# Kernel optimization log

Measured on AMD Instinct MI355X. Metric: run time of the kernel, lower is better.

Reference implementation:

```python
import jax, jax.numpy as jnp
import numpy as np

NC = 3
NA = 3
NO2D = NC + 5
BIN = 2
NO3D = BIN * 3 + 3
STRIDES = (8.0, 16.0, 32.0)
ANCHORS = np.array([[10, 13, 16, 30, 33, 23],
                    [30, 61, 62, 45, 59, 119],
                    [116, 90, 156, 198, 373, 326]], np.float32).reshape(3, NA, 2)
IN_CHES = (256, 512, 1024)
SIZES = ((80, 80), (40, 40), (20, 20))
BS = 8


def _conv(x, w, b, pad):
    y = jax.lax.conv_general_dilated(x, w, (1, 1), ((pad, pad), (pad, pad)),
                                     dimension_numbers=('NCHW', 'OIHW', 'NCHW'))
    return y + b[None, :, None, None]


def setup_inputs() -> dict:
    key = jax.random.key(0)
    d = {}
    k = [0]
    def nk():
        k[0] += 1
        return jax.random.fold_in(key, k[0])
    for i, (c, (ny, nx)) in enumerate(zip(IN_CHES, SIZES)):
        d[f"f{i}"] = jax.random.normal(nk(), (BS, c, ny, nx), jnp.float32)
        d[f"w2a{i}"] = jax.random.normal(nk(), (c, c, 3, 3), jnp.float32) * 0.01
        d[f"b2a{i}"] = jnp.zeros((c,), jnp.float32)
        d[f"w2b{i}"] = jax.random.normal(nk(), (NA * NO2D, c, 1, 1), jnp.float32) * 0.01
        d[f"b2b{i}"] = jnp.zeros((NA * NO2D,), jnp.float32)
        d[f"w3a{i}"] = jax.random.normal(nk(), (c, c, 3, 3), jnp.float32) * 0.01
        d[f"b3a{i}"] = jnp.zeros((c,), jnp.float32)
        d[f"w3b{i}"] = jax.random.normal(nk(), (NA * NO3D, c, 1, 1), jnp.float32) * 0.01
        d[f"b3b{i}"] = jnp.zeros((NA * NO3D,), jnp.float32)
    return d


def _decode(feats, params):
    anchors = jnp.asarray(ANCHORS)  # [L, NA, 2]
    preds = []
    for i in range(3):
        x = feats[i]
        w2a, b2a, w2b, b2b, w3a, b3a, w3b, b3b = params[i]
        # detection heads: 3x3 conv -> 1x1 conv
        h2 = _conv(_conv(x, w2a, b2a, 1), w2b, b2b, 0)  # [bs, na*NO2D, ny, nx]
        h3 = _conv(_conv(x, w3a, b3a, 1), w3b, b3b, 0)  # [bs, na*NO3D, ny, nx]
        bs, _, ny, nx = h2.shape
        h2 = h2.reshape(bs, NA, NO2D, ny, nx).transpose(0, 1, 3, 4, 2)  # [bs,na,ny,nx,NO2D]
        h3 = h3.reshape(bs, NA, NO3D, ny, nx).transpose(0, 1, 3, 4, 2).reshape(bs, -1, NO3D)
        # 2d decode
        p2 = jax.nn.sigmoid(h2)
        yv, xv = jnp.meshgrid(jnp.arange(ny, dtype=jnp.float32),
                              jnp.arange(nx, dtype=jnp.float32), indexing='ij')
        grid = jnp.stack((xv, yv), -1)[None, None]  # [1,1,ny,nx,2]
        xy = (p2[..., 0:2] * 2.0 - 0.5 + grid) * STRIDES[i]
        wh = (p2[..., 2:4] * 2.0) ** 2 * anchors[i][None, :, None, None, :]
        p2 = jnp.concatenate([xy, wh, p2[..., 4:]], -1).reshape(bs, -1, NO2D)
        # 3d decode: bin confidences raw, bin orients L2-normalized, dims sigmoid*2-1
        bins = h3[..., :BIN]
        orient = h3[..., BIN:3 * BIN].reshape(bs, -1, BIN, 2)
        norm = jnp.maximum(jnp.linalg.norm(orient, axis=-1, keepdims=True), 1e-12)
        orient = (orient / norm).reshape(bs, -1, BIN * 2)
        dims = jax.nn.sigmoid(h3[..., -3:]) * 2.0 - 1.0
        p3 = jnp.concatenate([bins, orient, dims], -1)
        preds.append(jnp.concatenate([p2, p3], -1))
    return jnp.concatenate(preds, 1)  # [bs, 25200, NO2D+NO3D]


def reference(f0, f1, f2,
              w2a0, b2a0, w2b0, b2b0, w3a0, b3a0, w3b0, b3b0,
              w2a1, b2a1, w2b1, b2b1, w3a1, b3a1, w3b1, b3b1,
              w2a2, b2a2, w2b2, b2b2, w3a2, b3a2, w3b2, b3b2):
    feats = (f0, f1, f2)
    params = ((w2a0, b2a0, w2b0, b2b0, w3a0, b3a0, w3b0, b3b0),
              (w2a1, b2a1, w2b1, b2b1, w3a1, b3a1, w3b1, b3b1),
              (w2a2, b2a2, w2b2, b2b2, w3a2, b3a2, w3b2, b3b2))
    return _decode(feats, params)
```

## Files before the change

kernel.cpp:

```cpp
#include <hip/hip_runtime.h>
#include <hip/hip_bf16.h>
#include <cstddef>
#include <cstdint>
#include <climits>

#define TOT_ANCH 25200

typedef __bf16 bf16x8 __attribute__((ext_vector_type(8)));
typedef float f32x4 __attribute__((ext_vector_type(4)));

__device__ __forceinline__ float sig_(float x) { return 1.0f / (1.0f + __expf(-x)); }

__device__ __forceinline__ short f2bf(float v) {
  return (short)__builtin_bit_cast(unsigned short, __float2bfloat16(v));
}
__device__ __forceinline__ float bf2f(short v) {
  unsigned int u = ((unsigned int)(unsigned short)v) << 16;
  return __builtin_bit_cast(float, u);
}
__device__ __forceinline__ bf16x8 as_bf16x8(int4 v) { return __builtin_bit_cast(bf16x8, v); }

__device__ __forceinline__ void gload_lds16(const void* g, void* l) {
  __builtin_amdgcn_global_load_lds((const __attribute__((address_space(1))) void*)g,
                                   (__attribute__((address_space(3))) void*)l, 16, 0, 0);
}

__device__ const float d_anch[3][3][2] = {
    {{10.f, 13.f}, {16.f, 30.f}, {33.f, 23.f}},
    {{30.f, 61.f}, {62.f, 45.f}, {59.f, 119.f}},
    {{116.f, 90.f}, {156.f, 198.f}, {373.f, 326.f}}};

struct TrP {
  const float* f; short* fb; int C, HW, ptiles, c32, blk0;
};
struct WtP {
  const float* w; short* dst; long CC, MC, off0; int blk0;
};
struct WcP {
  const float* w2b; const float* w3b; short* wc; int csh2, blk0;
};
struct ConvP {
  const short* fb; const short* wt; const float* bA; const float* bB; short* h;
  int C, H, W, HW, Ng, nb_m, nwg, mfast, blk0;
};
struct DeP {
  const short* h; const short* wc; const float* bb2; const float* bb3;
  int C2, H, W, b0, loff, ptiles, lvl, blk0; float stride;
};

__global__ __launch_bounds__(256) void aux_mega(TrP T0, TrP T1, TrP T2,
                                                WtP J0, WtP J1, WtP J2,
                                                WtP J3, WtP J4, WtP J5, int wt_blk0) {
  __shared__ short tile[32][33];
  int bid = blockIdx.x;
  if (bid >= wt_blk0) {
    WtP J = bid >= J5.blk0 ? J5 : bid >= J4.blk0 ? J4 : bid >= J3.blk0 ? J3 :
            bid >= J2.blk0 ? J2 : bid >= J1.blk0 ? J1 : J0;
    long oi = (long)(bid - J.blk0) * 256 + threadIdx.x;
    if (oi >= J.CC) return;
#pragma unroll
    for (int t = 0; t < 9; ++t) J.dst[t * J.MC + J.off0 + oi] = f2bf(J.w[oi * 9 + t]);
    return;
  }
  TrP T = bid >= T2.blk0 ? T2 : (bid >= T1.blk0 ? T1 : T0);
  int l = bid - T.blk0;
  const int pt = l % T.ptiles; l /= T.ptiles;
  const int cg = l % T.c32;
  const int b = l / T.c32;
  const int p0 = pt * 32, c0 = cg * 32, HW = T.HW, C = T.C;
  const int t = threadIdx.x;
  {
    int cl = t >> 3, pl = (t & 7) * 4;
    int pr = p0 + pl;
    if (pr > HW - 4) pr = HW - 4;
    const float4 v = *(const float4*)(T.f + ((long)b * C + c0 + cl) * HW + pr);
    tile[cl][pl + 0] = f2bf(v.x);
    tile[cl][pl + 1] = f2bf(v.y);
    tile[cl][pl + 2] = f2bf(v.z);
    tile[cl][pl + 3] = f2bf(v.w);
  }
  __syncthreads();
  {
    int pl = t >> 3, cl = (t & 7) * 4;
    int pp = p0 + pl;
    if (pp < HW) {
      int k = pl >> 2;
      int start = p0 + 4 * k;
      if (start > HW - 4) start = HW - 4;
      int col = (start - p0) + (pp - start);
      short4 o;
      o.x = tile[cl + 0][col];
      o.y = tile[cl + 1][col];
      o.z = tile[cl + 2][col];
      o.w = tile[cl + 3][col];
      *(short4*)(T.fb + ((long)b * HW + pp) * C + c0 + cl) = o;
    }
  }
}

__global__ __launch_bounds__(256) void wc_prep(WcP K0, WcP K1, WcP K2) {
  int bid = blockIdx.x;
  WcP K = bid >= K2.blk0 ? K2 : (bid >= K1.blk0 ? K1 : K0);
  int idx = (bid - K.blk0) * 256 + threadIdx.x;
  const int C2 = 1 << K.csh2;
  if (idx >= 64 * C2) return;
  const int row = idx >> K.csh2;
  const int c = idx & (C2 - 1);
  const int C = C2 >> 1;
  float v = 0.f;
  if (row < 24) {
    if (c < C) v = K.w2b[row * C + c];
  } else if (row < 51) {
    if (c >= C) v = K.w3b[(row - 24) * C + (c - C)];
  }
  K.wc[idx] = f2bf(v);
}

__global__ __launch_bounds__(512) void conv3x3_mega(ConvP P0, ConvP P1, ConvP P2,
                                                    const short* zbuf) {
  __shared__ __align__(16) short As[2][2][256 * 32];
  __shared__ __align__(16) short Xs[2][2][256 * 32];

  int bid = blockIdx.x;
  ConvP P = bid >= P2.blk0 ? P2 : (bid >= P1.blk0 ? P1 : P0);
  const int C = P.C, H = P.H, W = P.W, HW = P.HW, Ng = P.Ng;
  const int nb_m = P.nb_m, nwg = P.nwg;

  const int orig = bid - P.blk0;
  int wg;
  if (nwg & 7) wg = orig;
  else { const int q = nwg >> 3; wg = (orig & 7) * q + (orig >> 3); }
  int m, n;
  if (P.mfast) { m = wg % nb_m; n = wg / nb_m; }
  else         { const int nb_n = nwg / nb_m; n = wg % nb_n; m = wg / nb_n; }
  const int mt0 = m * 256;
  const int nt0 = n * 256;
  const int M2 = nb_m * 256;

  const int tid = threadIdx.x;
  const int lane = tid & 63;
  const int wave = tid >> 6;
  const int wm = wave >> 2;
  const int wn = wave & 3;

  const int srow0 = tid >> 2;
  const int swzc = ((tid & 3) ^ ((tid >> 3) & 3)) * 8;
  int xs_x[2], xs_y[2], xs_vld[2];
  long xs_base[2], as_base[2];
#pragma unroll
  for (int r = 0; r < 2; ++r) {
    int row = r * 128 + srow0;
    int nn = nt0 + row;
    int vld = nn < Ng;
    int nnc = vld ? nn : 0;
    int b = nnc / HW; int p = nnc - b * HW;
    int y = p / W;    int x = p - y * W;
    xs_x[r] = x; xs_y[r] = y; xs_vld[r] = vld;
    xs_base[r] = (long)((b * H + y) * W + x) * C + swzc;
    as_base[r] = (long)(mt0 + row) * C + swzc;
  }

  f32x4 acc[8][4];
#pragma unroll
  for (int a_ = 0; a_ < 8; ++a_)
#pragma unroll
    for (int b_ = 0; b_ < 4; ++b_) acc[a_][b_] = (f32x4){0.f, 0.f, 0.f, 0.f};

  const int nkb = C >> 6;
  const int nkt = nkb * 9;
  const long MC = (long)M2 * C;
  const short* gzb = zbuf + swzc;

  auto SA = [&](int db, int kh, const short* wtap, int kb64) {
#pragma unroll
    for (int r = 0; r < 2; ++r)
      gload_lds16(wtap + as_base[r] + kb64 + kh * 32,
                  (char*)&As[db][kh][0] + r * 8192 + tid * 16);
  };
  auto SX = [&](int db, int kh, int dy, int dx, int doff) {
#pragma unroll
    for (int r = 0; r < 2; ++r) {
      bool ok = xs_vld[r] && ((unsigned)(xs_y[r] + dy) < (unsigned)H) &&
                ((unsigned)(xs_x[r] + dx) < (unsigned)W);
      const short* gx = ok ? P.fb + xs_base[r] + doff + kh * 32 : gzb;
      gload_lds16(gx, (char*)&Xs[db][kh][0] + r * 8192 + tid * 16);
    }
  };

  {
    const int doff0 = (-W - 1) * C;
    SA(0, 0, P.wt, 0);
    SX(0, 0, -1, -1, doff0);
    SA(0, 1, P.wt, 0);
    SX(0, 1, -1, -1, doff0);
  }

  int ntt = 1, nkb64 = 0;
  for (int kt = 0; kt < nkt; ++kt) {
    const int cur = kt & 1;
    const int nxt = cur ^ 1;
    const bool hasn = (kt + 1) < nkt;
    const int td3 = ntt / 3;
    const int dyn = td3 - 1, dxn = ntt - td3 * 3 - 1;
    const int doffn = (dyn * W + dxn) * C + nkb64;
    const short* wtapn = P.wt + (long)ntt * MC;

    bf16x8 xf[4];
#pragma unroll
    for (int ph = 0; ph < 4; ++ph) {
      const int ks = ph >> 1, mh = ph & 1;
      if (mh == 0) {
        asm volatile("s_waitcnt vmcnt(4)" ::: "memory");
        __builtin_amdgcn_sched_barrier(0);
        __builtin_amdgcn_s_barrier();
      }
      if (hasn) {
        if (ph == 0)      SA(nxt, 0, wtapn, nkb64);
        else if (ph == 1) SX(nxt, 0, dyn, dxn, doffn);
        else if (ph == 2) SA(nxt, 1, wtapn, nkb64);
        else              SX(nxt, 1, dyn, dxn, doffn);
      }
      const char* Ah = (const char*)&As[cur][ks][0];
      const char* Xh = (const char*)&Xs[cur][ks][0];
      if (mh == 0) {
#pragma unroll
        for (int nf = 0; nf < 4; ++nf) {
          int rl = wn * 64 + nf * 16 + (lane & 15);
          int c = (lane >> 4) ^ ((rl >> 1) & 3);
          xf[nf] = as_bf16x8(*(const int4*)(Xh + rl * 64 + c * 16));
        }
      }
      bf16x8 af[4];
#pragma unroll
      for (int mf = 0; mf < 4; ++mf) {
        int rl = wm * 128 + mh * 64 + mf * 16 + (lane & 15);
        int c = (lane >> 4) ^ ((rl >> 1) & 3);
        af[mf] = as_bf16x8(*(const int4*)(Ah + rl * 64 + c * 16));
      }
      asm volatile("s_waitcnt lgkmcnt(0)" ::: "memory");
      __builtin_amdgcn_sched_barrier(0);
      __builtin_amdgcn_s_setprio(1);
#pragma unroll
      for (int mf = 0; mf < 4; ++mf)
#pragma unroll
        for (int nf = 0; nf < 4; ++nf)
          acc[mh * 4 + mf][nf] = __builtin_amdgcn_mfma_f32_16x16x32_bf16(
              af[mf], xf[nf], acc[mh * 4 + mf][nf], 0, 0, 0);
      __builtin_amdgcn_s_setprio(0);
    }
    if (++ntt == 9) { ntt = 0; nkb64 += 64; }
  }

  long nbase[4]; int nok[4];
#pragma unroll
  for (int nf = 0; nf < 4; ++nf) {
    int nn = nt0 + wn * 64 + nf * 16 + (lane & 15);
    nok[nf] = nn < Ng;
    int nnc = nok[nf] ? nn : 0;
    int nb = nnc / HW;
    int np = nnc - nb * HW;
    nbase[nf] = ((long)nb * HW + np) * M2;
  }
#pragma unroll
  for (int g = 0; g < 8; ++g) {
    int co0 = mt0 + wm * 128 + (g >> 2) * 64 + (g & 3) * 16 + (lane >> 4) * 4;
    float bv[4];
#pragma unroll
    for (int rg = 0; rg < 4; ++rg) {
      int co = co0 + rg;
      bv[rg] = co < C ? P.bA[co] : P.bB[co - C];
    }
#pragma unroll
    for (int nf = 0; nf < 4; ++nf) {
      if (nok[nf]) {
        short4 o;
        o.x = f2bf(acc[g][nf][0] + bv[0]);
        o.y = f2bf(acc[g][nf][1] + bv[1]);
        o.z = f2bf(acc[g][nf][2] + bv[2]);
        o.w = f2bf(acc[g][nf][3] + bv[3]);
        *(short4*)(P.h + nbase[nf] + co0) = o;
      }
    }
  }
}

__global__ __launch_bounds__(256) void decode_v3(DeP D0, DeP D1, DeP D2,
                                                 float* __restrict__ out) {
  __shared__ __align__(16) short htileT[32][136];
  __shared__ __align__(16) short Wtile[64][136];
  __shared__ float otile[32][52];
  int bid = blockIdx.x;
  DeP D = bid >= D2.blk0 ? D2 : (bid >= D1.blk0 ? D1 : D0);
  int l = bid - D.blk0;
  const int pt = l % D.ptiles;
  const int bl = l / D.ptiles;
  const int C2 = D.C2, H = D.H, W = D.W, HW = H * W;
  const int t = threadIdx.x;
  const int lane = t & 63;
  const int wv = t >> 6;
  const int p0 = pt * 32;

  const short* hB = D.h + (long)bl * HW * C2;

  f32x4 acc[2];
  acc[0] = (f32x4){0.f, 0.f, 0.f, 0.f};
  acc[1] = (f32x4){0.f, 0.f, 0.f, 0.f};

  const int rounds = C2 >> 7;
  for (int rd = 0; rd < rounds; ++rd) {
    const int c0 = rd << 7;
#pragma unroll
    for (int r = 0; r < 2; ++r) {
      int idx = r * 256 + t;
      int px = idx >> 4, kc = idx & 15;
      int p = p0 + px;
      int pc = p < HW ? p : HW - 1;
      int4 v = *(const int4*)(hB + (long)pc * C2 + c0 + kc * 8);
      *(int4*)&htileT[px][kc * 8] = v;
    }
#pragma unroll
    for (int r = 0; r < 4; ++r) {
      int idx = r * 256 + t;
      int row = idx >> 4, kc = idx & 15;
      int4 v = *(const int4*)(D.wc + (long)row * C2 + c0 + kc * 8);
      *(int4*)&Wtile[row][kc * 8] = v;
    }
    __syncthreads();
#pragma unroll
    for (int st = 0; st < 4; ++st) {
      const int k0 = st * 32 + (lane >> 4) * 8;
      bf16x8 af = as_bf16x8(*(const int4*)&Wtile[wv * 16 + (lane & 15)][k0]);
#pragma unroll
      for (int nf = 0; nf < 2; ++nf) {
        bf16x8 xf = as_bf16x8(*(const int4*)&htileT[nf * 16 + (lane & 15)][k0]);
        acc[nf] = __builtin_amdgcn_mfma_f32_16x16x32_bf16(af, xf, acc[nf], 0, 0, 0);
      }
    }
    __syncthreads();
  }

#pragma unroll
  for (int nf = 0; nf < 2; ++nf) {
    int px = nf * 16 + (lane & 15);
#pragma unroll
    for (int rg = 0; rg < 4; ++rg) {
      int row = wv * 16 + (lane >> 4) * 4 + rg;
      if (row < 51) otile[px][row] = acc[nf][rg];
    }
  }
  __syncthreads();

  if (t < 96) {
    const int pxx = t / 3, a = t - (t / 3) * 3;
    const int p = p0 + pxx;
    if (p < HW) {
      float* o = out + ((size_t)(D.b0 + bl) * TOT_ANCH + D.loff + (size_t)a * HW + p) * 17;
      {
        const int y = p / W, x = p - (p / W) * W;
        float h0 = otile[pxx][a * 8 + 0] + D.bb2[a * 8 + 0];
        float h1 = otile[pxx][a * 8 + 1] + D.bb2[a * 8 + 1];
        float h2 = otile[pxx][a * 8 + 2] + D.bb2[a * 8 + 2];
        float h3 = otile[pxx][a * 8 + 3] + D.bb2[a * 8 + 3];
        float s0 = sig_(h0);
        float s1 = sig_(h1);
        float sw = sig_(h2) * 2.f;
        float sh = sig_(h3) * 2.f;
        o[0] = (s0 * 2.f - 0.5f + (float)x) * D.stride;
        o[1] = (s1 * 2.f - 0.5f + (float)y) * D.stride;
        o[2] = sw * sw * d_anch[D.lvl][a][0];
        o[3] = sh * sh * d_anch[D.lvl][a][1];
        o[4] = sig_(otile[pxx][a * 8 + 4] + D.bb2[a * 8 + 4]);
        o[5] = sig_(otile[pxx][a * 8 + 5] + D.bb2[a * 8 + 5]);
        o[6] = sig_(otile[pxx][a * 8 + 6] + D.bb2[a * 8 + 6]);
        o[7] = sig_(otile[pxx][a * 8 + 7] + D.bb2[a * 8 + 7]);
      }
      {
        float v0 = otile[pxx][24 + a * 9 + 0] + D.bb3[a * 9 + 0];
        float v1 = otile[pxx][24 + a * 9 + 1] + D.bb3[a * 9 + 1];
        float v2 = otile[pxx][24 + a * 9 + 2] + D.bb3[a * 9 + 2];
        float v3 = otile[pxx][24 + a * 9 + 3] + D.bb3[a * 9 + 3];
        float v4 = otile[pxx][24 + a * 9 + 4] + D.bb3[a * 9 + 4];
        float v5 = otile[pxx][24 + a * 9 + 5] + D.bb3[a * 9 + 5];
        float v6 = otile[pxx][24 + a * 9 + 6] + D.bb3[a * 9 + 6];
        float v7 = otile[pxx][24 + a * 9 + 7] + D.bb3[a * 9 + 7];
        float v8 = otile[pxx][24 + a * 9 + 8] + D.bb3[a * 9 + 8];
        float n0 = fmaxf(sqrtf(v2 * v2 + v3 * v3), 1e-12f);
        float n1 = fmaxf(sqrtf(v4 * v4 + v5 * v5), 1e-12f);
        o[8] = v0;
        o[9] = v1;
        o[10] = v2 / n0;
        o[11] = v3 / n0;
        o[12] = v4 / n1;
        o[13] = v5 / n1;
        o[14] = sig_(v6) * 2.f - 1.f;
        o[15] = sig_(v7) * 2.f - 1.f;
        o[16] = sig_(v8) * 2.f - 1.f;
      }
    }
  }
}


static inline size_t al256(size_t x) { return (x + 255) & ~(size_t)255; }

extern "C" void kernel_launch(void* const* d_in, const int* in_sizes, int n_in,
                              void* d_out, int out_size, void* d_ws, size_t ws_size,
                              hipStream_t stream) {
  (void)in_sizes; (void)n_in; (void)out_size;
  char* ws = (char*)d_ws;
  float* out = (float*)d_out;

  hipMemsetAsync(ws, 0, 256, stream);
  const short* zb = (const short*)ws;

  struct Lvl { int C, H, W, loff; float stride; };
  const Lvl L[3] = {{256, 80, 80, 0, 8.f}, {512, 40, 40, 19200, 16.f},
                    {1024, 20, 20, 24000, 32.f}};
  const int B = 8;
  const int ord[3] = {2, 1, 0};

  const float* f_[3]; const float *w2a_[3], *b2a_[3], *w2b_[3], *b2b_[3];
  const float *w3a_[3], *b3a_[3], *w3b_[3], *b3b_[3];
  int HW_[3], ptiles_[3], c32_[3], nbm_[3], mfast_[3], csh2_[3];
  long CC_[3];
  size_t fbB_[3], wtB_[3], hB_[3], wcB_[3];
  for (int i = 0; i < 3; ++i) {
    f_[i]   = (const float*)d_in[9 * i + 0];
    w2a_[i] = (const float*)d_in[9 * i + 1];
    b2a_[i] = (const float*)d_in[9 * i + 2];
    w2b_[i] = (const float*)d_in[9 * i + 3];
    b2b_[i] = (const float*)d_in[9 * i + 4];
    w3a_[i] = (const float*)d_in[9 * i + 5];
    b3a_[i] = (const float*)d_in[9 * i + 6];
    w3b_[i] = (const float*)d_in[9 * i + 7];
    b3b_[i] = (const float*)d_in[9 * i + 8];
    const int C = L[i].C;
    HW_[i] = L[i].H * L[i].W;
    ptiles_[i] = (HW_[i] + 31) / 32;
    c32_[i] = C / 32;
    nbm_[i] = (2 * C) / 256;
    CC_[i] = (long)C * C;
    csh2_[i] = (C == 256) ? 9 : (C == 512) ? 10 : 11;
    fbB_[i] = (size_t)B * HW_[i] * C * 2;
    wtB_[i] = (size_t)36 * CC_[i];
    hB_[i]  = (size_t)B * HW_[i] * 2 * C * 2;
    wcB_[i] = (size_t)64 * 2 * C * 2;
    mfast_[i] = ((size_t)B * HW_[i] * C >= (size_t)18 * CC_[i]) ? 1 : 0;
  }

  size_t off = 256;
  size_t fb_o[3], wt_o[3], h_o[3], wc_o[3];
  for (int i = 0; i < 3; ++i) { fb_o[i] = off; off += al256(fbB_[i]); }
  for (int i = 0; i < 3; ++i) { wt_o[i] = off; off += al256(wtB_[i]); }
  for (int i = 0; i < 3; ++i) { wc_o[i] = off; off += al256(wcB_[i]); }
  for (int i = 0; i < 3; ++i) { h_o[i] = off; off += al256(hB_[i]); }

  if (off <= ws_size) {
    short* fb[3]; short* wtb[3]; short* hb[3]; short* wcb[3];
    for (int i = 0; i < 3; ++i) {
      fb[i] = (short*)(ws + fb_o[i]);
      wtb[i] = (short*)(ws + wt_o[i]);
      hb[i] = (short*)(ws + h_o[i]);
      wcb[i] = (short*)(ws + wc_o[i]);
    }
    TrP T[3]; int tb = 0;
    for (int i = 0; i < 3; ++i) {
      T[i] = TrP{f_[i], fb[i], L[i].C, HW_[i], ptiles_[i], c32_[i], tb};
      tb += ptiles_[i] * c32_[i] * B;
    }
    WtP J[6]; int jb = tb;
    for (int i = 0; i < 3; ++i) {
      J[2 * i]     = WtP{w2a_[i], wtb[i], CC_[i], 2 * CC_[i], 0, jb};
      jb += (int)(CC_[i] / 256);
      J[2 * i + 1] = WtP{w3a_[i], wtb[i], CC_[i], 2 * CC_[i], CC_[i], jb};
      jb += (int)(CC_[i] / 256);
    }
    aux_mega<<<jb, 256, 0, stream>>>(T[0], T[1], T[2], J[0], J[1], J[2], J[3], J[4],
                                     J[5], tb);
    WcP K[3]; int kb = 0;
    for (int i = 0; i < 3; ++i) {
      K[i] = WcP{w2b_[i], w3b_[i], wcb[i], csh2_[i], kb};
      kb += (64 * 2 * L[i].C) / 256;
    }
    wc_prep<<<kb, 256, 0, stream>>>(K[0], K[1], K[2]);

    ConvP P[3]; int cb = 0;
    for (int k = 0; k < 3; ++k) {
      const int i = ord[k];
      const int Ng = B * HW_[i];
      const int ntn = (Ng + 255) / 256;
      const int nwg = ntn * nbm_[i];
      P[k] = ConvP{fb[i], wtb[i], b2a_[i], b3a_[i], hb[i],
                   L[i].C, L[i].H, L[i].W, HW_[i], Ng, nbm_[i], nwg, mfast_[i], cb};
      cb += nwg;
    }
    conv3x3_mega<<<cb, 512, 0, stream>>>(P[0], P[1], P[2], zb);

    DeP D[3]; int db = 0;
    for (int k = 0; k < 3; ++k) {
      const int i = ord[k];
      D[k] = DeP{hb[i], wcb[i], b2b_[i], b3b_[i], 2 * L[i].C, L[i].H, L[i].W,
                 0, L[i].loff, ptiles_[i], i, db, L[i].stride};
      db += ptiles_[i] * B;
    }
    decode_v3<<<db, 256, 0, stream>>>(D[0], D[1], D[2], out);
    return;
  }

  for (int i = 0; i < 3; ++i) {
    const int C = L[i].C, HW = HW_[i];
    int Bg = B;
    for (int cand = 1; cand <= 8; cand <<= 1) {
      int bg = B / cand;
      size_t need = 256 + al256((size_t)bg * HW * C * 2) + al256(wtB_[i]) +
                    al256(wcB_[i]) + (size_t)bg * HW * 2 * C * 2;
      if (need <= ws_size) { Bg = bg; break; }
    }
    size_t fo = 256;
    size_t wo = fo + al256((size_t)Bg * HW * C * 2);
    size_t co = wo + al256(wtB_[i]);
    size_t ho = co + al256(wcB_[i]);
    short* fb = (short*)(ws + fo);
    short* wtb = (short*)(ws + wo);
    short* wcb = (short*)(ws + co);
    short* hb = (short*)(ws + ho);

    TrP TZ{};
    WtP J0 = WtP{w2a_[i], wtb, CC_[i], 2 * CC_[i], 0, 0};
    WtP J1 = WtP{w3a_[i], wtb, CC_[i], 2 * CC_[i], CC_[i], (int)(CC_[i] / 256)};
    WtP JX = J1; JX.blk0 = INT_MAX;
    aux_mega<<<(int)(2 * CC_[i] / 256), 256, 0, stream>>>(TZ, TZ, TZ, J0, J1, JX, JX,
                                                          JX, JX, 0);
    WcP K0 = WcP{w2b_[i], w3b_[i], wcb, csh2_[i], 0};
    WcP KX = K0; KX.blk0 = INT_MAX;
    wc_prep<<<(64 * 2 * C) / 256, 256, 0, stream>>>(K0, KX, KX);

    const int nbg = B / Bg;
    for (int g = 0; g < nbg; ++g) {
      const int b0 = g * Bg;
      TrP T0 = TrP{f_[i] + (size_t)b0 * C * HW, fb, C, HW, ptiles_[i], c32_[i], 0};
      TrP TX = T0; TX.blk0 = INT_MAX;
      WtP JZ{}; JZ.blk0 = INT_MAX;
      aux_mega<<<ptiles_[i] * c32_[i] * Bg, 256, 0, stream>>>(T0, TX, TX, JZ, JZ, JZ,
                                                              JZ, JZ, JZ, INT_MAX);

      const int Ng = Bg * HW;
      const int ntn = (Ng + 255) / 256;
      const int nwg = ntn * nbm_[i];
      ConvP Pc = ConvP{fb, wtb, b2a_[i], b3a_[i], hb, C, L[i].H, L[i].W, HW,
                       Ng, nbm_[i], nwg, mfast_[i], 0};
      ConvP PX = Pc; PX.blk0 = INT_MAX;
      conv3x3_mega<<<nwg, 512, 0, stream>>>(Pc, PX, PX, zb);

      DeP D0 = DeP{hb, wcb, b2b_[i], b3b_[i], 2 * C, L[i].H, L[i].W,
                   b0, L[i].loff, ptiles_[i], i, 0, L[i].stride};
      DeP DX = D0; DX.blk0 = INT_MAX;
      decode_v3<<<ptiles_[i] * Bg, 256, 0, stream>>>(D0, DX, DX, out);
    }
  }
}
```

Baseline: 469.2 us.

## Use zero-padded feature layout to drop bounds checks in conv gather

Stores the bf16 NHWC features in a buffer padded by one pixel on each side and adds a block range in the aux kernel that zeroes the border, so the 3x3 conv gather loads without per-tap bounds checks or a zero-buffer redirect. The conv main loop is also restructured to issue all next-stage loads at the top and synchronise once per iteration with __syncthreads, replacing the phase-interleaved vmcnt waits. Launch bounds now request two blocks per CU. The padded buffer uses slightly more memory. Coarser synchronisation can lose the load/compute overlap the old schedule had.

```diff
diff --git a/kernel.cpp b/kernel.cpp
--- a/kernel.cpp
+++ b/kernel.cpp
@@ -31,7 +31,10 @@
     {{116.f, 90.f}, {156.f, 198.f}, {373.f, 326.f}}};
 
 struct TrP {
-  const float* f; short* fb; int C, HW, ptiles, c32, blk0;
+  const float* f; short* fb; int C, H, W, HW, ptiles, c32, blk0;
+};
+struct ZP {
+  short* fb; int C, H, W, nb, items, blk0;
 };
 struct WtP {
   const float* w; short* dst; long CC, MC, off0; int blk0;
@@ -49,8 +52,10 @@
 };
 
 __global__ __launch_bounds__(256) void aux_mega(TrP T0, TrP T1, TrP T2,
+                                                ZP Z0, ZP Z1, ZP Z2,
                                                 WtP J0, WtP J1, WtP J2,
-                                                WtP J3, WtP J4, WtP J5, int wt_blk0) {
+                                                WtP J3, WtP J4, WtP J5,
+                                                int zb_blk0, int wt_blk0) {
   __shared__ short tile[32][33];
   int bid = blockIdx.x;
   if (bid >= wt_blk0) {
@@ -62,12 +67,35 @@
     for (int t = 0; t < 9; ++t) J.dst[t * J.MC + J.off0 + oi] = f2bf(J.w[oi * 9 + t]);
     return;
   }
+  if (bid >= zb_blk0) {
+    ZP Z = bid >= Z2.blk0 ? Z2 : (bid >= Z1.blk0 ? Z1 : Z0);
+    int idx = (bid - Z.blk0) * 256 + threadIdx.x;
+    if (idx >= Z.items) return;
+    const int c8 = Z.C >> 3;
+    int ci = idx % c8;
+    int rem = idx / c8;
+    int b = rem / Z.nb;
+    int k = rem - b * Z.nb;
+    const int W2 = Z.W + 2;
+    int y, x;
+    if (k < W2) { y = 0; x = k; }
+    else if (k < 2 * W2) { y = Z.H + 1; x = k - W2; }
+    else {
+      int kk = k - 2 * W2;
+      if (kk < Z.H) { y = 1 + kk; x = 0; }
+      else { y = 1 + kk - Z.H; x = W2 - 1; }
+    }
+    short* dst = Z.fb + (((long)b * (Z.H + 2) + y) * W2 + x) * Z.C + ci * 8;
+    *(int4*)dst = (int4){0, 0, 0, 0};
+    return;
+  }
   TrP T = bid >= T2.blk0 ? T2 : (bid >= T1.blk0 ? T1 : T0);
   int l = bid - T.blk0;
   const int pt = l % T.ptiles; l /= T.ptiles;
   const int cg = l % T.c32;
   const int b = l / T.c32;
   const int p0 = pt * 32, c0 = cg * 32, HW = T.HW, C = T.C;
+  const int H = T.H, W = T.W;
   const int t = threadIdx.x;
   {
     int cl = t >> 3, pl = (t & 7) * 4;
@@ -93,7 +121,8 @@
       o.y = tile[cl + 1][col];
       o.z = tile[cl + 2][col];
       o.w = tile[cl + 3][col];
-      *(short4*)(T.fb + ((long)b * HW + pp) * C + c0 + cl) = o;
+      int y = pp / W, x = pp - y * W;
+      *(short4*)(T.fb + (((long)b * (H + 2) + y + 1) * (W + 2) + x + 1) * C + c0 + cl) = o;
     }
   }
 }
@@ -116,8 +145,7 @@
   K.wc[idx] = f2bf(v);
 }
 
-__global__ __launch_bounds__(512) void conv3x3_mega(ConvP P0, ConvP P1, ConvP P2,
-                                                    const short* zbuf) {
+__global__ __launch_bounds__(512, 2) void conv3x3_mega(ConvP P0, ConvP P1, ConvP P2) {
   __shared__ __align__(16) short As[2][2][256 * 32];
   __shared__ __align__(16) short Xs[2][2][256 * 32];
 
@@ -125,11 +153,16 @@
   ConvP P = bid >= P2.blk0 ? P2 : (bid >= P1.blk0 ? P1 : P0);
   const int C = P.C, H = P.H, W = P.W, HW = P.HW, Ng = P.Ng;
   const int nb_m = P.nb_m, nwg = P.nwg;
+  const int W2 = W + 2;
 
   const int orig = bid - P.blk0;
   int wg;
-  if (nwg & 7) wg = orig;
-  else { const int q = nwg >> 3; wg = (orig & 7) * q + (orig >> 3); }
+  if (nwg & 7) {
+    wg = orig;
+  } else {
+    const int q = nwg >> 3;
+    wg = (orig & 7) * q + (orig >> 3);
+  }
   int m, n;
   if (P.mfast) { m = wg % nb_m; n = wg / nb_m; }
   else         { const int nb_n = nwg / nb_m; n = wg % nb_n; m = wg / nb_n; }
@@ -145,18 +178,15 @@
 
   const int srow0 = tid >> 2;
   const int swzc = ((tid & 3) ^ ((tid >> 3) & 3)) * 8;
-  int xs_x[2], xs_y[2], xs_vld[2];
   long xs_base[2], as_base[2];
 #pragma unroll
   for (int r = 0; r < 2; ++r) {
     int row = r * 128 + srow0;
     int nn = nt0 + row;
-    int vld = nn < Ng;
-    int nnc = vld ? nn : 0;
+    int nnc = nn < Ng ? nn : 0;
     int b = nnc / HW; int p = nnc - b * HW;
     int y = p / W;    int x = p - y * W;
-    xs_x[r] = x; xs_y[r] = y; xs_vld[r] = vld;
-    xs_base[r] = (long)((b * H + y) * W + x) * C + swzc;
+    xs_base[r] = (((long)b * (H + 2) + y + 1) * W2 + x + 1) * C + swzc;
     as_base[r] = (long)(mt0 + row) * C + swzc;
   }
 
@@ -169,7 +199,6 @@
   const int nkb = C >> 6;
   const int nkt = nkb * 9;
   const long MC = (long)M2 * C;
-  const short* gzb = zbuf + swzc;
 
   auto SA = [&](int db, int kh, const short* wtap, int kb64) {
 #pragma unroll
@@ -177,49 +206,42 @@
       gload_lds16(wtap + as_base[r] + kb64 + kh * 32,
                   (char*)&As[db][kh][0] + r * 8192 + tid * 16);
   };
-  auto SX = [&](int db, int kh, int dy, int dx, int doff) {
-#pragma unroll
-    for (int r = 0; r < 2; ++r) {
-      bool ok = xs_vld[r] && ((unsigned)(xs_y[r] + dy) < (unsigned)H) &&
-                ((unsigned)(xs_x[r] + dx) < (unsigned)W);
-      const short* gx = ok ? P.fb + xs_base[r] + doff + kh * 32 : gzb;
-      gload_lds16(gx, (char*)&Xs[db][kh][0] + r * 8192 + tid * 16);
-    }
+  auto SX = [&](int db, int kh, int doff) {
+#pragma unroll
+    for (int r = 0; r < 2; ++r)
+      gload_lds16(P.fb + xs_base[r] + doff + kh * 32,
+                  (char*)&Xs[db][kh][0] + r * 8192 + tid * 16);
   };
 
   {
-    const int doff0 = (-W - 1) * C;
+    const int doff0 = (-W2 - 1) * C;
     SA(0, 0, P.wt, 0);
-    SX(0, 0, -1, -1, doff0);
     SA(0, 1, P.wt, 0);
-    SX(0, 1, -1, -1, doff0);
+    SX(0, 0, doff0);
+    SX(0, 1, doff0);
+    __syncthreads();
   }
 
   int ntt = 1, nkb64 = 0;
   for (int kt = 0; kt < nkt; ++kt) {
     const int cur = kt & 1;
     const int nxt = cur ^ 1;
-    const bool hasn = (kt + 1) < nkt;
-    const int td3 = ntt / 3;
-    const int dyn = td3 - 1, dxn = ntt - td3 * 3 - 1;
-    const int doffn = (dyn * W + dxn) * C + nkb64;
-    const short* wtapn = P.wt + (long)ntt * MC;
+
+    if (kt + 1 < nkt) {
+      const int td3 = ntt / 3;
+      const int dyn = td3 - 1, dxn = ntt - td3 * 3 - 1;
+      const int doffn = (dyn * W2 + dxn) * C + nkb64;
+      const short* wtapn = P.wt + (long)ntt * MC;
+      SA(nxt, 0, wtapn, nkb64);
+      SA(nxt, 1, wtapn, nkb64);
+      SX(nxt, 0, doffn);
+      SX(nxt, 1, doffn);
+    }
 
     bf16x8 xf[4];
 #pragma unroll
     for (int ph = 0; ph < 4; ++ph) {
       const int ks = ph >> 1, mh = ph & 1;
-      if (mh == 0) {
-        asm volatile("s_waitcnt vmcnt(4)" ::: "memory");
-        __builtin_amdgcn_sched_barrier(0);
-        __builtin_amdgcn_s_barrier();
-      }
-      if (hasn) {
-        if (ph == 0)      SA(nxt, 0, wtapn, nkb64);
-        else if (ph == 1) SX(nxt, 0, dyn, dxn, doffn);
-        else if (ph == 2) SA(nxt, 1, wtapn, nkb64);
-        else              SX(nxt, 1, dyn, dxn, doffn);
-      }
       const char* Ah = (const char*)&As[cur][ks][0];
       const char* Xh = (const char*)&Xs[cur][ks][0];
       if (mh == 0) {
@@ -237,8 +259,6 @@
         int c = (lane >> 4) ^ ((rl >> 1) & 3);
         af[mf] = as_bf16x8(*(const int4*)(Ah + rl * 64 + c * 16));
       }
-      asm volatile("s_waitcnt lgkmcnt(0)" ::: "memory");
-      __builtin_amdgcn_sched_barrier(0);
       __builtin_amdgcn_s_setprio(1);
 #pragma unroll
       for (int mf = 0; mf < 4; ++mf)
@@ -248,6 +268,7 @@
               af[mf], xf[nf], acc[mh * 4 + mf][nf], 0, 0, 0);
       __builtin_amdgcn_s_setprio(0);
     }
+    __syncthreads();
     if (++ntt == 9) { ntt = 0; nkb64 += 64; }
   }
 
@@ -410,9 +431,6 @@
   char* ws = (char*)d_ws;
   float* out = (float*)d_out;
 
-  hipMemsetAsync(ws, 0, 256, stream);
-  const short* zb = (const short*)ws;
-
   struct Lvl { int C, H, W, loff; float stride; };
   const Lvl L[3] = {{256, 80, 80, 0, 8.f}, {512, 40, 40, 19200, 16.f},
                     {1024, 20, 20, 24000, 32.f}};
@@ -421,7 +439,7 @@
 
   const float* f_[3]; const float *w2a_[3], *b2a_[3], *w2b_[3], *b2b_[3];
   const float *w3a_[3], *b3a_[3], *w3b_[3], *b3b_[3];
-  int HW_[3], ptiles_[3], c32_[3], nbm_[3], mfast_[3], csh2_[3];
+  int HW_[3], ptiles_[3], c32_[3], nbm_[3], mfast_[3], csh2_[3], nbrd_[3];
   long CC_[3];
   size_t fbB_[3], wtB_[3], hB_[3], wcB_[3];
   for (int i = 0; i < 3; ++i) {
@@ -434,14 +452,15 @@
     b3a_[i] = (const float*)d_in[9 * i + 6];
     w3b_[i] = (const float*)d_in[9 * i + 7];
     b3b_[i] = (const float*)d_in[9 * i + 8];
-    const int C = L[i].C;
-    HW_[i] = L[i].H * L[i].W;
+    const int C = L[i].C, H = L[i].H, W = L[i].W;
+    HW_[i] = H * W;
     ptiles_[i] = (HW_[i] + 31) / 32;
     c32_[i] = C / 32;
     nbm_[i] = (2 * C) / 256;
     CC_[i] = (long)C * C;
     csh2_[i] = (C == 256) ? 9 : (C == 512) ? 10 : 11;
-    fbB_[i] = (size_t)B * HW_[i] * C * 2;
+    nbrd_[i] = 2 * (W + 2) + 2 * H;
+    fbB_[i] = (size_t)B * (H + 2) * (W + 2) * C * 2;
     wtB_[i] = (size_t)36 * CC_[i];
     hB_[i]  = (size_t)B * HW_[i] * 2 * C * 2;
     wcB_[i] = (size_t)64 * 2 * C * 2;
@@ -465,18 +484,24 @@
     }
     TrP T[3]; int tb = 0;
     for (int i = 0; i < 3; ++i) {
-      T[i] = TrP{f_[i], fb[i], L[i].C, HW_[i], ptiles_[i], c32_[i], tb};
+      T[i] = TrP{f_[i], fb[i], L[i].C, L[i].H, L[i].W, HW_[i], ptiles_[i], c32_[i], tb};
       tb += ptiles_[i] * c32_[i] * B;
     }
-    WtP J[6]; int jb = tb;
+    ZP Z[3]; int zbb = tb;
+    for (int i = 0; i < 3; ++i) {
+      int items = B * nbrd_[i] * (L[i].C >> 3);
+      Z[i] = ZP{fb[i], L[i].C, L[i].H, L[i].W, nbrd_[i], items, zbb};
+      zbb += (items + 255) / 256;
+    }
+    WtP J[6]; int jb = zbb;
     for (int i = 0; i < 3; ++i) {
       J[2 * i]     = WtP{w2a_[i], wtb[i], CC_[i], 2 * CC_[i], 0, jb};
       jb += (int)(CC_[i] / 256);
       J[2 * i + 1] = WtP{w3a_[i], wtb[i], CC_[i], 2 * CC_[i], CC_[i], jb};
       jb += (int)(CC_[i] / 256);
     }
-    aux_mega<<<jb, 256, 0, stream>>>(T[0], T[1], T[2], J[0], J[1], J[2], J[3], J[4],
-                                     J[5], tb);
+    aux_mega<<<jb, 256, 0, stream>>>(T[0], T[1], T[2], Z[0], Z[1], Z[2],
+                                     J[0], J[1], J[2], J[3], J[4], J[5], tb, zbb);
     WcP K[3]; int kb = 0;
     for (int i = 0; i < 3; ++i) {
       K[i] = WcP{w2b_[i], w3b_[i], wcb[i], csh2_[i], kb};
@@ -494,7 +519,7 @@
                    L[i].C, L[i].H, L[i].W, HW_[i], Ng, nbm_[i], nwg, mfast_[i], cb};
       cb += nwg;
     }
-    conv3x3_mega<<<cb, 512, 0, stream>>>(P[0], P[1], P[2], zb);
+    conv3x3_mega<<<cb, 512, 0, stream>>>(P[0], P[1], P[2]);
 
     DeP D[3]; int db = 0;
     for (int k = 0; k < 3; ++k) {
@@ -508,16 +533,16 @@
   }
 
   for (int i = 0; i < 3; ++i) {
-    const int C = L[i].C, HW = HW_[i];
+    const int C = L[i].C, H = L[i].H, W = L[i].W, HW = HW_[i];
     int Bg = B;
     for (int cand = 1; cand <= 8; cand <<= 1) {
       int bg = B / cand;
-      size_t need = 256 + al256((size_t)bg * HW * C * 2) + al256(wtB_[i]) +
-                    al256(wcB_[i]) + (size_t)bg * HW * 2 * C * 2;
+      size_t need = 256 + al256((size_t)bg * (H + 2) * (W + 2) * C * 2) +
+                    al256(wtB_[i]) + al256(wcB_[i]) + (size_t)bg * HW * 2 * C * 2;
       if (need <= ws_size) { Bg = bg; break; }
     }
     size_t fo = 256;
-    size_t wo = fo + al256((size_t)Bg * HW * C * 2);
+    size_t wo = fo + al256((size_t)Bg * (H + 2) * (W + 2) * C * 2);
     size_t co = wo + al256(wtB_[i]);
     size_t ho = co + al256(wcB_[i]);
     short* fb = (short*)(ws + fo);
@@ -525,12 +550,12 @@
     short* wcb = (short*)(ws + co);
     short* hb = (short*)(ws + ho);
 
-    TrP TZ{};
+    TrP TZ{}; ZP ZZ{}; ZZ.blk0 = INT_MAX;
     WtP J0 = WtP{w2a_[i], wtb, CC_[i], 2 * CC_[i], 0, 0};
     WtP J1 = WtP{w3a_[i], wtb, CC_[i], 2 * CC_[i], CC_[i], (int)(CC_[i] / 256)};
     WtP JX = J1; JX.blk0 = INT_MAX;
-    aux_mega<<<(int)(2 * CC_[i] / 256), 256, 0, stream>>>(TZ, TZ, TZ, J0, J1, JX, JX,
-                                                          JX, JX, 0);
+    aux_mega<<<(int)(2 * CC_[i] / 256), 256, 0, stream>>>(TZ, TZ, TZ, ZZ, ZZ, ZZ,
+                                                          J0, J1, JX, JX, JX, JX, 0, 0);
     WcP K0 = WcP{w2b_[i], w3b_[i], wcb, csh2_[i], 0};
     WcP KX = K0; KX.blk0 = INT_MAX;
     wc_prep<<<(64 * 2 * C) / 256, 256, 0, stream>>>(K0, KX, KX);
@@ -538,21 +563,26 @@
     const int nbg = B / Bg;
     for (int g = 0; g < nbg; ++g) {
       const int b0 = g * Bg;
-      TrP T0 = TrP{f_[i] + (size_t)b0 * C * HW, fb, C, HW, ptiles_[i], c32_[i], 0};
+      TrP T0 = TrP{f_[i] + (size_t)b0 * C * HW, fb, C, H, W, HW, ptiles_[i], c32_[i], 0};
       TrP TX = T0; TX.blk0 = INT_MAX;
+      int trb = ptiles_[i] * c32_[i] * Bg;
+      int items = Bg * nbrd_[i] * (C >> 3);
+      ZP Z0 = ZP{fb, C, H, W, nbrd_[i], items, trb};
+      ZP ZX = Z0; ZX.blk0 = INT_MAX;
+      int zblk = (items + 255) / 256;
       WtP JZ{}; JZ.blk0 = INT_MAX;
-      aux_mega<<<ptiles_[i] * c32_[i] * Bg, 256, 0, stream>>>(T0, TX, TX, JZ, JZ, JZ,
-                                                              JZ, JZ, JZ, INT_MAX);
+      aux_mega<<<trb + zblk, 256, 0, stream>>>(T0, TX, TX, Z0, ZX, ZX, JZ, JZ, JZ,
+                                               JZ, JZ, JZ, trb, INT_MAX);
 
       const int Ng = Bg * HW;
       const int ntn = (Ng + 255) / 256;
       const int nwg = ntn * nbm_[i];
-      ConvP Pc = ConvP{fb, wtb, b2a_[i], b3a_[i], hb, C, L[i].H, L[i].W, HW,
+      ConvP Pc = ConvP{fb, wtb, b2a_[i], b3a_[i], hb, C, H, W, HW,
                        Ng, nbm_[i], nwg, mfast_[i], 0};
       ConvP PX = Pc; PX.blk0 = INT_MAX;
-      conv3x3_mega<<<nwg, 512, 0, stream>>>(Pc, PX, PX, zb);
-
-      DeP D0 = DeP{hb, wcb, b2b_[i], b3b_[i], 2 * C, L[i].H, L[i].W,
+      conv3x3_mega<<<nwg, 512, 0, stream>>>(Pc, PX, PX);
+
+      DeP D0 = DeP{hb, wcb, b2b_[i], b3b_[i], 2 * C, H, W,
                    b0, L[i].loff, ptiles_[i], i, 0, L[i].stride};
       DeP DX = D0; DX.blk0 = INT_MAX;
       decode_v3<<<ptiles_[i] * Bg, 256, 0, stream>>>(D0, DX, DX, out);
```

New measurement: 442.1 us. 5.8% less time.
